# Performance work log

Hardware: AMD Instinct MI355X
Metric: run time of the kernel (lower is better)

The kernel has to match this reference:

```python
import jax, jax.numpy as jnp
import numpy as np

N = 16384      # number of nodes (pos rows)
S = 16384      # number of src nodes (src_pos rows)
E = 262144     # number of edges (COO entries)
D = 512        # embed_dim
H = 8          # num_heads
HD = D // H    # head_dim = 64
HID = 1024     # mlp hidden
MLP_IN = D + 3 * H  # 536
EPS = 1e-5


def layer_norm(x, g, b):
    mu = jnp.mean(x, axis=-1, keepdims=True)
    var = jnp.mean((x - mu) ** 2, axis=-1, keepdims=True)
    return (x - mu) * jax.lax.rsqrt(var + EPS) * g + b


def setup_inputs() -> dict:
    key = jax.random.key(0)
    ks = jax.random.split(key, 20)
    s = 1.0 / np.sqrt(D)
    sh = 1.0 / np.sqrt(HID)
    return {
        "x": jax.random.normal(ks[0], (N, D), jnp.float32),
        "Wq": jax.random.uniform(ks[1], (D, D), jnp.float32, -s, s),
        "bq": jnp.zeros((D,), jnp.float32),
        "Wk": jax.random.uniform(ks[2], (D, D), jnp.float32, -s, s),
        "bk": jnp.zeros((D,), jnp.float32),
        "g_att": jnp.ones((D,), jnp.float32),
        "b_att": jnp.zeros((D,), jnp.float32),
        "g_mlp": jnp.ones((D,), jnp.float32),
        "b_mlp": jnp.zeros((D,), jnp.float32),
        "W_in": jax.random.uniform(ks[3], (HID, MLP_IN), jnp.float32, -s, s),
        "b_in": jnp.zeros((HID,), jnp.float32),
        "W_out": jax.random.uniform(ks[4], (D, HID), jnp.float32, -sh, sh),
        "b_out": jnp.zeros((D,), jnp.float32),
        "att_bias": jax.random.normal(ks[5], (H, E), jnp.float32),
        "dist": jax.random.uniform(ks[6], (E,), jnp.float32, 0.5, 6.0),
        "pos": jax.random.normal(ks[7], (N, 3), jnp.float32),
        "src_pos": jax.random.normal(ks[8], (S, 3), jnp.float32),
        "row_index": jax.random.randint(ks[9], (E,), 0, N),
        "src_index": jax.random.randint(ks[10], (E,), 0, S),
        "org_to_src": jax.random.randint(ks[11], (S,), 0, N),
    }


def reference(x, Wq, bq, Wk, bk, g_att, b_att, g_mlp, b_mlp, W_in, b_in,
              W_out, b_out, att_bias, dist, pos, src_pos,
              row_index, src_index, org_to_src):
    n = x.shape[0]
    z = layer_norm(x, g_att, b_att)
    q = (z @ Wq.T + bq).reshape(n, H, HD)          # [N,H,hd]
    k = (z @ Wk.T + bk).reshape(n, H, HD)          # [N,H,hd]
    k_src = k[org_to_src]                          # [S,H,hd]
    # per-edge masked logits: q[row] . k_src[col] / sqrt(hd) + bias
    qe = q[row_index]                              # [E,H,hd]
    ke = k_src[src_index]                          # [E,H,hd]
    logits = jnp.einsum('ehd,ehd->eh', qe, ke) / jnp.sqrt(jnp.float32(HD))
    logits = logits + att_bias.T                   # [E,H]
    # segment (per-row) softmax over incident edges
    m = jax.ops.segment_max(logits, row_index, num_segments=n)
    p = jnp.exp(logits - m[row_index])
    den = jax.ops.segment_sum(p, row_index, num_segments=n)
    att = p / den[row_index]                       # [E,H]
    inv = jnp.where(dist == 0, 0.0, 1.0 / dist)[:, None]
    att = att * inv
    # sparse bmm: feat[h,row] += att * src_pos[col]; rowsum for centering
    sp = src_pos[src_index]                        # [E,3]
    feat = jax.ops.segment_sum(att[:, :, None] * sp[:, None, :],
                               row_index, num_segments=n)   # [N,H,3]
    rowsum = jax.ops.segment_sum(att, row_index, num_segments=n)  # [N,H]
    feat = feat - rowsum[:, :, None] * pos[:, None, :]
    feat = feat.reshape(n, H * 3)
    z2 = layer_norm(x, g_mlp, b_mlp)
    h = jax.nn.gelu(jnp.concatenate([z2, feat], axis=-1) @ W_in.T + b_in)
    return x + (h @ W_out.T + b_out)
```

## Files before the change

kernel.cpp:

```cpp
#include <hip/hip_runtime.h>
#include <math.h>


typedef unsigned short u16;
typedef __attribute__((ext_vector_type(8))) short bf16x8;
typedef __attribute__((ext_vector_type(4))) float f32x4;
typedef __attribute__((ext_vector_type(2))) float f32x2;

constexpr int N_NODES = 16384;
constexpr int E_EDGES = 262144;
constexpr int D = 512;
constexpr int KIN = 576;

constexpr size_t OFF_ZATT = 0;
constexpr size_t OFF_ZCAT = 16777216;
constexpr size_t OFF_WQK  = 35651584;
constexpr size_t OFF_BQK  = 36700160;
constexpr size_t OFF_WIN  = 36704256;
constexpr size_t OFF_WOUT = 37883904;
constexpr size_t OFF_QK   = 38932480;
constexpr size_t OFF_BKT  = 55775232;
constexpr size_t OFF_HBF  = 59969536;
constexpr size_t OFF_CNTP = 93523968;

static __device__ __forceinline__ u16 f2bf(float f) {
  union { float f; unsigned int u; } v; v.f = f;
  unsigned int u = v.u;
  u = u + 0x7FFFu + ((u >> 16) & 1u);
  return (u16)(u >> 16);
}
static __device__ __forceinline__ void gload16(const u16* g, u16* l) {
  __builtin_amdgcn_global_load_lds(
      (const __attribute__((address_space(1))) unsigned int*)g,
      (__attribute__((address_space(3))) unsigned int*)l, 16, 0, 0);
}

__global__ __launch_bounds__(256) void prep_edges(
    const int* __restrict__ row_index,
    const float* __restrict__ att_bias, const float* __restrict__ dist,
    const float* __restrict__ src_pos, const int* __restrict__ src_index,
    const int* __restrict__ org_to_src,
    int* __restrict__ cntp, int* __restrict__ bucket, float* __restrict__ rec)
{
  const int gid = blockIdx.x * 256 + threadIdx.x;
  const int r = row_index[gid];
  const int s = src_index[gid];
  const float dv = dist[gid];
  float4 q0, q1, q2, q3;
  q0.x = att_bias[gid];
  q0.y = att_bias[(size_t)1 * E_EDGES + gid];
  q0.z = att_bias[(size_t)2 * E_EDGES + gid];
  q0.w = att_bias[(size_t)3 * E_EDGES + gid];
  q1.x = att_bias[(size_t)4 * E_EDGES + gid];
  q1.y = att_bias[(size_t)5 * E_EDGES + gid];
  q1.z = att_bias[(size_t)6 * E_EDGES + gid];
  q1.w = att_bias[(size_t)7 * E_EDGES + gid];
  q2.x = (dv == 0.f) ? 0.f : 1.f / dv;
  q2.y = src_pos[(size_t)s * 3 + 0];
  q2.z = src_pos[(size_t)s * 3 + 1];
  q2.w = src_pos[(size_t)s * 3 + 2];
  q3.x = __int_as_float(org_to_src[s]);
  q3.y = 0.f; q3.z = 0.f; q3.w = 0.f;
  float4* rg = (float4*)(rec + (size_t)gid * 16);
  rg[0] = q0; rg[1] = q1; rg[2] = q2; rg[3] = q3;
  const int p = atomicAdd(&cntp[r * 16], 1);
  if (p < 64) bucket[(size_t)r * 64 + p] = gid;
}

__global__ __launch_bounds__(256) void prep_wln(
    const float* __restrict__ Wq, const float* __restrict__ Wk,
    const float* __restrict__ bq, const float* __restrict__ bk,
    const float* __restrict__ W_in, const float* __restrict__ W_out,
    u16* __restrict__ wqk, float* __restrict__ bqk,
    u16* __restrict__ win, u16* __restrict__ wout,
    const float* __restrict__ x,
    const float* __restrict__ g1, const float* __restrict__ b1,
    const float* __restrict__ g2, const float* __restrict__ b2,
    u16* __restrict__ zatt, u16* __restrict__ zcat)
{
  if (blockIdx.x < 2304) {
    const int gid = blockIdx.x * 256 + threadIdx.x;
    if (gid < 512 * 1024) {
      wqk[gid]  = f2bf(gid < 512 * 512 ? Wq[gid] : Wk[gid - 512 * 512]);
      wout[gid] = f2bf(W_out[gid]);
    }
    if (gid < 1024 * KIN) {
      const int r = gid / KIN, c = gid - r * KIN;
      win[gid] = f2bf(c < 536 ? W_in[r * 536 + c] : 0.f);
    }
    if (gid < 1024) bqk[gid] = gid < 512 ? bq[gid] : bk[gid - 512];
    return;
  }
  const int row = (blockIdx.x - 2304) * 4 + (threadIdx.x >> 6);
  const int l = threadIdx.x & 63;
  const float* xr = x + (size_t)row * D + l * 8;
  const float4 v0 = *(const float4*)(xr);
  const float4 v1 = *(const float4*)(xr + 4);
  float s  = v0.x + v0.y + v0.z + v0.w + v1.x + v1.y + v1.z + v1.w;
  float s2 = v0.x * v0.x + v0.y * v0.y + v0.z * v0.z + v0.w * v0.w
           + v1.x * v1.x + v1.y * v1.y + v1.z * v1.z + v1.w * v1.w;
#pragma unroll
  for (int m = 1; m < 64; m <<= 1) {
    s  += __shfl_xor(s, m, 64);
    s2 += __shfl_xor(s2, m, 64);
  }
  const float mu = s * (1.f / D);
  const float var = s2 * (1.f / D) - mu * mu;
  const float rs = rsqrtf(var + 1e-5f);
  const int c0 = l * 8;
  const float4 ga0 = *(const float4*)(g1 + c0), ga1 = *(const float4*)(g1 + c0 + 4);
  const float4 ba0 = *(const float4*)(b1 + c0), ba1 = *(const float4*)(b1 + c0 + 4);
  const float4 gm0 = *(const float4*)(g2 + c0), gm1 = *(const float4*)(g2 + c0 + 4);
  const float4 bm0 = *(const float4*)(b2 + c0), bm1 = *(const float4*)(b2 + c0 + 4);
  float n[8] = { (v0.x - mu) * rs, (v0.y - mu) * rs, (v0.z - mu) * rs, (v0.w - mu) * rs,
                 (v1.x - mu) * rs, (v1.y - mu) * rs, (v1.z - mu) * rs, (v1.w - mu) * rs };
  const float ga[8] = { ga0.x, ga0.y, ga0.z, ga0.w, ga1.x, ga1.y, ga1.z, ga1.w };
  const float ba[8] = { ba0.x, ba0.y, ba0.z, ba0.w, ba1.x, ba1.y, ba1.z, ba1.w };
  const float gm[8] = { gm0.x, gm0.y, gm0.z, gm0.w, gm1.x, gm1.y, gm1.z, gm1.w };
  const float bm[8] = { bm0.x, bm0.y, bm0.z, bm0.w, bm1.x, bm1.y, bm1.z, bm1.w };
  bf16x8 za, zc;
#pragma unroll
  for (int i = 0; i < 8; ++i) {
    za[i] = (short)f2bf(n[i] * ga[i] + ba[i]);
    zc[i] = (short)f2bf(n[i] * gm[i] + bm[i]);
  }
  *(bf16x8*)(zatt + (size_t)row * D + c0) = za;
  *(bf16x8*)(zcat + (size_t)row * KIN + c0) = zc;
  if (l < 32) ((unsigned int*)(zcat + (size_t)row * KIN + D))[l] = 0;
}


#define MM_BLK(AF, BF, NB) do {                                               \
  __builtin_amdgcn_s_setprio(1);                                              \
  _Pragma("unroll")                                                           \
  for (int mi = 0; mi < 8; ++mi) {                                            \
    acc[mi][NB]     = __builtin_amdgcn_mfma_f32_16x16x32_bf16(AF[mi], BF[0], acc[mi][NB], 0, 0, 0);     \
    acc[mi][NB + 1] = __builtin_amdgcn_mfma_f32_16x16x32_bf16(AF[mi], BF[1], acc[mi][NB + 1], 0, 0, 0); \
  }                                                                           \
  __builtin_amdgcn_s_setprio(0);                                              \
} while (0)

template <int EPI>
__global__ __launch_bounds__(512, 2) void gemm256(
    const u16* __restrict__ A, const u16* __restrict__ B,
    const float* __restrict__ bias,
    void* __restrict__ Cout, int M, int Nn, int K)
{
  extern __shared__ __align__(16) u16 lds[];
  const int tid = threadIdx.x;
  const int lane = tid & 63;
  const int wave = tid >> 6;
  const int wave_m = wave >> 2;
  const int wave_n = wave & 3;
  const int m0 = blockIdx.x * 256;
  const int n0 = blockIdx.y * 256;
  const int fr = lane & 15;
  const int fq = lane >> 4;
  const int NT = K >> 6;
  const int sw = (fq ^ ((fr >> 1) & 3)) * 8;

  f32x4 acc[8][4];
#pragma unroll
  for (int i = 0; i < 8; ++i)
#pragma unroll
    for (int j = 0; j < 4; ++j) acc[i][j] = 0.f;

  auto stageA = [&](int slot, int ktile, int kh) {
    u16* base = lds + slot * 8192;
    const int kb = ktile * 64 + kh * 32;
#pragma unroll
    for (int r = 0; r < 2; ++r) {
      const int g = r * 512 + tid;
      const int row = g >> 2;
      const int gs = (g & 3) ^ ((row >> 1) & 3);
      gload16(A + (size_t)(m0 + row) * K + kb + gs * 8,
              base + (r * 512 + wave * 64) * 8);
    }
  };
  auto stageB = [&](int slot, int ktile, int kh) {
    u16* base = lds + 32768 + slot * 8192;
    const int kb = ktile * 64 + kh * 32;
#pragma unroll
    for (int r = 0; r < 2; ++r) {
      const int g = r * 512 + tid;
      const int row = g >> 2;
      const int gs = (g & 3) ^ ((row >> 1) & 3);
      gload16(B + (size_t)(n0 + row) * K + kb + gs * 8,
              base + (r * 512 + wave * 64) * 8);
    }
  };
  auto ldA = [&](bf16x8 (&af)[8], int slot) {
    const u16* p = lds + slot * 8192 + (wave_m * 128 + fr) * 32 + sw;
#pragma unroll
    for (int mi = 0; mi < 8; ++mi)
      af[mi] = *(const bf16x8*)(p + mi * 16 * 32);
  };
  auto ldB = [&](bf16x8 (&bf)[2], int slot, int nh) {
    const u16* p = lds + 32768 + slot * 8192 + (wave_n * 64 + nh * 32 + fr) * 32 + sw;
    bf[0] = *(const bf16x8*)(p);
    bf[1] = *(const bf16x8*)(p + 16 * 32);
  };

  stageA(0, 0, 0); stageB(0, 0, 0);
  stageA(1, 0, 1); stageB(1, 0, 1);
  stageA(2, 1, 0); stageB(2, 1, 0);
  stageA(3, 1, 1);
  asm volatile("s_waitcnt vmcnt(10)" ::: "memory");
  __builtin_amdgcn_s_barrier();
  asm volatile("" ::: "memory");

  bf16x8 af[8], bf0[2], bf1[2];
  for (int t = 0; t < NT; ++t) {
    const int sa0 = (2 * t) & 3,  sa1 = (2 * t + 1) & 3;
    const int sb1n = (2 * t + 3) & 3;
    const int t1 = (t + 1 >= NT) ? t + 1 - NT : t + 1;
    const int t2 = (t + 2 >= NT) ? t + 2 - NT : t + 2;

    ldA(af, sa0); ldB(bf0, sa0, 0);
    stageB(sb1n, t1, 1);
    __builtin_amdgcn_s_barrier();
    asm volatile("" ::: "memory");
    MM_BLK(af, bf0, 0);
    __builtin_amdgcn_s_barrier();
    asm volatile("" ::: "memory");
    ldB(bf1, sa0, 1);
    stageA(sa0, t2, 0);
    __builtin_amdgcn_s_barrier();
    asm volatile("" ::: "memory");
    MM_BLK(af, bf1, 2);
    asm volatile("s_waitcnt vmcnt(10)" ::: "memory");
    __builtin_amdgcn_s_barrier();
    asm volatile("" ::: "memory");
    ldA(af, sa1); ldB(bf0, sa1, 0);
    stageB(sa0, t2, 0);
    __builtin_amdgcn_s_barrier();
    asm volatile("" ::: "memory");
    MM_BLK(af, bf0, 0);
    __builtin_amdgcn_s_barrier();
    asm volatile("" ::: "memory");
    ldB(bf1, sa1, 1);
    stageA(sa1, t2, 1);
    __builtin_amdgcn_s_barrier();
    asm volatile("" ::: "memory");
    MM_BLK(af, bf1, 2);
    asm volatile("s_waitcnt vmcnt(10)" ::: "memory");
    __builtin_amdgcn_s_barrier();
    asm volatile("" ::: "memory");
  }
  asm volatile("s_waitcnt vmcnt(0)" ::: "memory");

#pragma unroll
  for (int mi = 0; mi < 8; ++mi) {
#pragma unroll
    for (int nj = 0; nj < 4; ++nj) {
      const int col = n0 + wave_n * 64 + nj * 16 + fr;
      const float bv = bias[col];
#pragma unroll
      for (int rr = 0; rr < 4; ++rr) {
        const int row = m0 + wave_m * 128 + mi * 16 + fq * 4 + rr;
        float v = acc[mi][nj][rr] + bv;
        if (EPI == 1) {
          const float nu = -1.5957691216057308f * (v + 0.044715f * v * v * v);
          const float sg = __builtin_amdgcn_rcpf(1.f + __expf(nu));
          ((u16*)Cout)[(size_t)row * Nn + col] = f2bf(v * sg);
        } else {
          const int pk = __builtin_amdgcn_cvt_pk_fp8_f32(v, v, 0, false);
          ((unsigned char*)Cout)[(size_t)row * Nn + col] = (unsigned char)(pk & 0xFF);
        }
      }
    }
  }
}

template <int EPI, int WPE>
__global__ __launch_bounds__(256, WPE) void gemm_nt(
    const u16* __restrict__ A, const u16* __restrict__ B,
    const float* __restrict__ bias, const float* __restrict__ resid,
    void* __restrict__ Cout, int M, int Nn, int K)
{
  constexpr int BM = 128, BN = 128, BK = 32;
  __shared__ __align__(16) u16 As[2 * BM * BK];
  __shared__ __align__(16) u16 Bs[2 * BN * BK];
  const int tid = threadIdx.x;
  const int lane = tid & 63;
  const int wave = tid >> 6;
  const int m0 = blockIdx.x * BM;
  const int n0 = blockIdx.y * BN;
  const int wm = (wave >> 1) * 64;
  const int wn = (wave & 1) * 64;
  const int fr = lane & 15;
  const int fq = lane >> 4;
  const int srow = lane >> 2;
  const int skoff = ((lane & 3) ^ ((srow >> 1) & 3)) * 8;
  const int sw = (fq ^ ((fr >> 1) & 3)) * 8;

  f32x4 acc[4][4];
#pragma unroll
  for (int i = 0; i < 4; ++i)
#pragma unroll
    for (int j = 0; j < 4; ++j) acc[i][j] = 0.f;

  for (int k0 = 0; k0 < K; k0 += 2 * BK) {
    __syncthreads();
#pragma unroll
    for (int t = 0; t < 2; ++t) {
#pragma unroll
      for (int r = 0; r < 2; ++r) {
        const int rowbase = r * 64 + wave * 16;
        gload16(A + (size_t)(m0 + rowbase + srow) * K + k0 + t * BK + skoff,
                As + t * (BM * BK) + rowbase * BK);
        gload16(B + (size_t)(n0 + rowbase + srow) * K + k0 + t * BK + skoff,
                Bs + t * (BM * BK) + rowbase * BK);
      }
    }
    __syncthreads();
#pragma unroll
    for (int t = 0; t < 2; ++t) {
      bf16x8 af[4], bfr[4];
#pragma unroll
      for (int mi = 0; mi < 4; ++mi)
        af[mi] = *(const bf16x8*)(As + t * (BM * BK) + (wm + mi * 16 + fr) * BK + sw);
#pragma unroll
      for (int ni = 0; ni < 4; ++ni)
        bfr[ni] = *(const bf16x8*)(Bs + t * (BM * BK) + (wn + ni * 16 + fr) * BK + sw);
#pragma unroll
      for (int mi = 0; mi < 4; ++mi)
#pragma unroll
        for (int ni = 0; ni < 4; ++ni)
          acc[mi][ni] = __builtin_amdgcn_mfma_f32_16x16x32_bf16(af[mi], bfr[ni], acc[mi][ni], 0, 0, 0);
    }
  }

#pragma unroll
  for (int mi = 0; mi < 4; ++mi) {
#pragma unroll
    for (int ni = 0; ni < 4; ++ni) {
      const int col = n0 + wn + ni * 16 + fr;
      const float bv = bias[col];
#pragma unroll
      for (int rr = 0; rr < 4; ++rr) {
        const int row = m0 + wm + mi * 16 + fq * 4 + rr;
        float v = acc[mi][ni][rr] + bv;
        if (EPI == 1) {
          const float nu = -1.5957691216057308f * (v + 0.044715f * v * v * v);
          const float sg = __builtin_amdgcn_rcpf(1.f + __expf(nu));
          ((u16*)Cout)[(size_t)row * Nn + col] = f2bf(v * sg);
        } else if (EPI == 2) {
          ((float*)Cout)[(size_t)row * Nn + col] = v + resid[(size_t)row * Nn + col];
        } else {
          const int pk = __builtin_amdgcn_cvt_pk_fp8_f32(v, v, 0, false);
          ((unsigned char*)Cout)[(size_t)row * Nn + col] = (unsigned char)(pk & 0xFF);
        }
      }
    }
  }
}

__global__ __launch_bounds__(256) void edge_csr(
    const unsigned char* __restrict__ qk8, const float* __restrict__ rec,
    const int* __restrict__ cntp, const int* __restrict__ bucket,
    const float* __restrict__ pos, u16* __restrict__ zcat)
{
  const int lane = threadIdx.x & 63;
  const int wave = threadIdx.x >> 6;
  const int row = blockIdx.x * 4 + wave;
  const int half = lane >> 5;
  const int sub = lane & 31;
  const int h = sub >> 2, j = sub & 3;
  const int deg = min(cntp[row * 16], 64);
  const int base = row * 64;

  const uint4 qv = *(const uint4*)(qk8 + (size_t)row * 1024 + sub * 16);
  float qf[16];
  {
    const unsigned int* qu = (const unsigned int*)&qv;
#pragma unroll
    for (int i = 0; i < 4; ++i) {
      const f32x2 lo = __builtin_amdgcn_cvt_pk_f32_fp8(qu[i], false);
      const f32x2 hi = __builtin_amdgcn_cvt_pk_f32_fp8(qu[i], true);
      qf[i * 4 + 0] = lo.x; qf[i * 4 + 1] = lo.y;
      qf[i * 4 + 2] = hi.x; qf[i * 4 + 3] = hi.y;
    }
  }

  float accA = 0.f, accB = 0.f;
  const int npair = (deg + 1) >> 1;

  bool ok0 = half < deg;
  int e0 = ok0 ? bucket[base + half] : 0;
  const float* r0 = rec + (size_t)e0 * 16;
  float bias0 = r0[h], invd0 = r0[8];
  float spA0 = (j >= 2) ? r0[7 + j] : 0.f;
  float spB0 = (j == 1) ? r0[11] : 0.f;
  uint4 kv0 = *(const uint4*)(qk8 + (size_t)__float_as_int(r0[12]) * 1024 + 512 + sub * 16);

  bool ok1 = 2 + half < deg;
  int e1 = ok1 ? bucket[base + 2 + half] : 0;
  const float* r1 = rec + (size_t)e1 * 16;
  float bias1 = r1[h], invd1 = r1[8];
  float spA1 = (j >= 2) ? r1[7 + j] : 0.f;
  float spB1 = (j == 1) ? r1[11] : 0.f;
  uint4 kv1 = *(const uint4*)(qk8 + (size_t)__float_as_int(r1[12]) * 1024 + 512 + sub * 16);

  bool ok2 = 4 + half < deg;
  int e2 = ok2 ? bucket[base + 4 + half] : 0;
  const float* r2p = rec + (size_t)e2 * 16;
  float bias2 = r2p[h], invd2 = r2p[8];
  float spA2 = (j >= 2) ? r2p[7 + j] : 0.f;
  float spB2 = (j == 1) ? r2p[11] : 0.f;
  int kr2 = __float_as_int(r2p[12]);

  bool ok3 = 6 + half < deg;
  int e3 = ok3 ? bucket[base + 6 + half] : 0;

  for (int i = 0; i < npair; ++i) {
    const uint4 kv2 = *(const uint4*)(qk8 + (size_t)kr2 * 1024 + 512 + sub * 16);
    const float* r3 = rec + (size_t)e3 * 16;
    const float bias3 = r3[h], invd3 = r3[8];
    const float spA3 = (j >= 2) ? r3[7 + j] : 0.f;
    const float spB3 = (j == 1) ? r3[11] : 0.f;
    const int kr3 = __float_as_int(r3[12]);
    const bool ok4 = 2 * (i + 4) + half < deg;
    const int e4 = ok4 ? bucket[base + 2 * (i + 4) + half] : 0;

    float p;
    {
      const unsigned int* ku = (const unsigned int*)&kv0;
      const f32x2 a0 = __builtin_amdgcn_cvt_pk_f32_fp8(ku[0], false);
      const f32x2 a1 = __builtin_amdgcn_cvt_pk_f32_fp8(ku[0], true);
      const f32x2 b0 = __builtin_amdgcn_cvt_pk_f32_fp8(ku[1], false);
      const f32x2 b1 = __builtin_amdgcn_cvt_pk_f32_fp8(ku[1], true);
      const f32x2 c0 = __builtin_amdgcn_cvt_pk_f32_fp8(ku[2], false);
      const f32x2 c1 = __builtin_amdgcn_cvt_pk_f32_fp8(ku[2], true);
      const f32x2 d0 = __builtin_amdgcn_cvt_pk_f32_fp8(ku[3], false);
      const f32x2 d1 = __builtin_amdgcn_cvt_pk_f32_fp8(ku[3], true);
      p = qf[0] * a0.x;
      p = fmaf(qf[1],  a0.y, p);  p = fmaf(qf[2],  a1.x, p);  p = fmaf(qf[3],  a1.y, p);
      p = fmaf(qf[4],  b0.x, p);  p = fmaf(qf[5],  b0.y, p);  p = fmaf(qf[6],  b1.x, p);
      p = fmaf(qf[7],  b1.y, p);  p = fmaf(qf[8],  c0.x, p);  p = fmaf(qf[9],  c0.y, p);
      p = fmaf(qf[10], c1.x, p);  p = fmaf(qf[11], c1.y, p);  p = fmaf(qf[12], d0.x, p);
      p = fmaf(qf[13], d0.y, p);  p = fmaf(qf[14], d1.x, p);  p = fmaf(qf[15], d1.y, p);
    }
    p += __shfl_xor(p, 1, 64);
    p += __shfl_xor(p, 2, 64);
    float pe = __expf(p * 0.125f + bias0);
    pe = ok0 ? pe : 0.f;
    const float w = pe * invd0;
    accA += (j == 0) ? pe : (j == 1) ? w : w * spA0;
    accB += w * spB0;

    ok0 = ok1; bias0 = bias1; invd0 = invd1; spA0 = spA1; spB0 = spB1; kv0 = kv1;
    ok1 = ok2; bias1 = bias2; invd1 = invd2; spA1 = spA2; spB1 = spB2; kv1 = kv2;
    ok2 = ok3; bias2 = bias3; invd2 = invd3; spA2 = spA3; spB2 = spB3; kr2 = kr3;
    ok3 = ok4; e3 = e4;
  }

  accA += __shfl_xor(accA, 32, 64);
  accB += __shfl_xor(accB, 32, 64);
  const int hb = h << 2;
  const float den  = __shfl(accA, hb + 0, 64);
  const float wsum = __shfl(accA, hb + 1, 64);
  const float wsp01 = __shfl(accA, hb + 2 + (j & 1), 64);
  const float wsp2  = __shfl(accB, hb + 1, 64);
  const float invd = (den != 0.f) ? 1.f / den : 0.f;
  const float rsum = wsum * invd;
  if (half == 0 && j < 3) {
    const float wspj = (j < 2) ? wsp01 : wsp2;
    zcat[(size_t)row * KIN + D + h * 3 + j] = f2bf(wspj * invd - rsum * pos[row * 3 + j]);
  }
}

extern "C" void kernel_launch(void* const* d_in, const int* in_sizes, int n_in,
                              void* d_out, int out_size, void* d_ws, size_t ws_size,
                              hipStream_t stream)
{
  const float* x        = (const float*)d_in[0];
  const float* Wq       = (const float*)d_in[1];
  const float* bq       = (const float*)d_in[2];
  const float* Wk       = (const float*)d_in[3];
  const float* bk       = (const float*)d_in[4];
  const float* g_att    = (const float*)d_in[5];
  const float* b_att    = (const float*)d_in[6];
  const float* g_mlp    = (const float*)d_in[7];
  const float* b_mlp    = (const float*)d_in[8];
  const float* W_in     = (const float*)d_in[9];
  const float* b_in     = (const float*)d_in[10];
  const float* W_out    = (const float*)d_in[11];
  const float* b_out    = (const float*)d_in[12];
  const float* att_bias = (const float*)d_in[13];
  const float* dist     = (const float*)d_in[14];
  const float* pos      = (const float*)d_in[15];
  const float* src_pos  = (const float*)d_in[16];
  const int* row_index  = (const int*)d_in[17];
  const int* src_index  = (const int*)d_in[18];
  const int* org_to_src = (const int*)d_in[19];

  char* ws = (char*)d_ws;
  u16*   zatt = (u16*)(ws + OFF_ZATT);
  u16*   zcat = (u16*)(ws + OFF_ZCAT);
  u16*   wqk  = (u16*)(ws + OFF_WQK);
  float* bqk  = (float*)(ws + OFF_BQK);
  u16*   win  = (u16*)(ws + OFF_WIN);
  u16*   wout = (u16*)(ws + OFF_WOUT);
  unsigned char* qk8 = (unsigned char*)(ws + OFF_QK);
  int*   bkt  = (int*)(ws + OFF_BKT);
  u16*   hbf  = (u16*)(ws + OFF_HBF);
  float* rec  = (float*)(ws + OFF_HBF);
  int*   cntp = (int*)(ws + OFF_CNTP);

  static bool s_attr = false;
  if (!s_attr) {
    hipFuncSetAttribute(reinterpret_cast<const void*>(&gemm256<4>),
                        hipFuncAttributeMaxDynamicSharedMemorySize, 131072);
    hipFuncSetAttribute(reinterpret_cast<const void*>(&gemm256<1>),
                        hipFuncAttributeMaxDynamicSharedMemorySize, 131072);
    s_attr = true;
  }

  hipMemsetAsync(ws + OFF_CNTP, 0, 16384 * 64, stream);

  prep_edges<<<E_EDGES / 256, 256, 0, stream>>>(
      row_index, att_bias, dist, src_pos, src_index, org_to_src, cntp, bkt, rec);
  prep_wln<<<2304 + N_NODES / 4, 256, 0, stream>>>(
      Wq, Wk, bq, bk, W_in, W_out, wqk, bqk, win, wout,
      x, g_att, b_att, g_mlp, b_mlp, zatt, zcat);
  gemm256<4><<<dim3(64, 4), 512, 131072, stream>>>(zatt, wqk, bqk, qk8, N_NODES, 1024, 512);
  edge_csr<<<N_NODES / 4, 256, 0, stream>>>(qk8, rec, cntp, bkt, pos, zcat);
  gemm256<1><<<dim3(64, 4), 512, 131072, stream>>>(zcat, win, b_in, hbf, N_NODES, 1024, KIN);
  gemm_nt<2, 2><<<dim3(128, 4), 256, 0, stream>>>(hbf, wout, b_out, x, d_out, N_NODES, 512, 1024);
}
```

Before: 256.5 us.

## Fuse MLP up and down projections into one kernel keeping hidden in LDS

Replaces the two separate MLP GEMM launches with a single kernel. Each 64-row block computes the GELU hidden activations into shared memory and then immediately multiplies by W_out, adding bias and residual. This avoids writing and re-reading the full bf16 hidden tensor through global memory and saves a launch. In exchange it uses about 144KB of LDS per block, which limits occupancy to one block per CU, and weight operands are streamed from global/L2 into registers without LDS staging.

```diff
diff --git a/kernel.cpp b/kernel.cpp
--- a/kernel.cpp
+++ b/kernel.cpp
@@ -20,7 +20,7 @@
 constexpr size_t OFF_WOUT = 37883904;
 constexpr size_t OFF_QK   = 38932480;
 constexpr size_t OFF_BKT  = 55775232;
-constexpr size_t OFF_HBF  = 59969536;
+constexpr size_t OFF_REC  = 59969536;
 constexpr size_t OFF_CNTP = 93523968;
 
 static __device__ __forceinline__ u16 f2bf(float f) {
@@ -129,7 +129,6 @@
   if (l < 32) ((unsigned int*)(zcat + (size_t)row * KIN + D))[l] = 0;
 }
 
-
 #define MM_BLK(AF, BF, NB) do {                                               \
   __builtin_amdgcn_s_setprio(1);                                              \
   _Pragma("unroll")                                                           \
@@ -272,88 +271,169 @@
   }
 }
 
-template <int EPI, int WPE>
-__global__ __launch_bounds__(256, WPE) void gemm_nt(
-    const u16* __restrict__ A, const u16* __restrict__ B,
-    const float* __restrict__ bias, const float* __restrict__ resid,
-    void* __restrict__ Cout, int M, int Nn, int K)
+__global__ __launch_bounds__(512, 2) void gemm23(
+    const u16* __restrict__ zcat, const u16* __restrict__ win,
+    const float* __restrict__ b_in, const u16* __restrict__ wout,
+    const float* __restrict__ b_out, const float* __restrict__ x,
+    float* __restrict__ out)
 {
-  constexpr int BM = 128, BN = 128, BK = 32;
-  __shared__ __align__(16) u16 As[2 * BM * BK];
-  __shared__ __align__(16) u16 Bs[2 * BN * BK];
+  extern __shared__ __align__(16) u16 lds[];
+  u16* As = lds;
+  u16* Hs = lds + 8192;
   const int tid = threadIdx.x;
   const int lane = tid & 63;
-  const int wave = tid >> 6;
-  const int m0 = blockIdx.x * BM;
-  const int n0 = blockIdx.y * BN;
-  const int wm = (wave >> 1) * 64;
-  const int wn = (wave & 1) * 64;
+  const int wv = tid >> 6;
   const int fr = lane & 15;
   const int fq = lane >> 4;
-  const int srow = lane >> 2;
-  const int skoff = ((lane & 3) ^ ((srow >> 1) & 3)) * 8;
-  const int sw = (fq ^ ((fr >> 1) & 3)) * 8;
-
-  f32x4 acc[4][4];
+  const int m0 = blockIdx.x * 64;
+
+  f32x4 acc[4][8];
 #pragma unroll
   for (int i = 0; i < 4; ++i)
 #pragma unroll
-    for (int j = 0; j < 4; ++j) acc[i][j] = 0.f;
-
-  for (int k0 = 0; k0 < K; k0 += 2 * BK) {
-    __syncthreads();
-#pragma unroll
-    for (int t = 0; t < 2; ++t) {
-#pragma unroll
-      for (int r = 0; r < 2; ++r) {
-        const int rowbase = r * 64 + wave * 16;
-        gload16(A + (size_t)(m0 + rowbase + srow) * K + k0 + t * BK + skoff,
-                As + t * (BM * BK) + rowbase * BK);
-        gload16(B + (size_t)(n0 + rowbase + srow) * K + k0 + t * BK + skoff,
-                Bs + t * (BM * BK) + rowbase * BK);
-      }
-    }
-    __syncthreads();
-#pragma unroll
-    for (int t = 0; t < 2; ++t) {
-      bf16x8 af[4], bfr[4];
-#pragma unroll
-      for (int mi = 0; mi < 4; ++mi)
-        af[mi] = *(const bf16x8*)(As + t * (BM * BK) + (wm + mi * 16 + fr) * BK + sw);
-#pragma unroll
-      for (int ni = 0; ni < 4; ++ni)
-        bfr[ni] = *(const bf16x8*)(Bs + t * (BM * BK) + (wn + ni * 16 + fr) * BK + sw);
-#pragma unroll
-      for (int mi = 0; mi < 4; ++mi)
-#pragma unroll
-        for (int ni = 0; ni < 4; ++ni)
-          acc[mi][ni] = __builtin_amdgcn_mfma_f32_16x16x32_bf16(af[mi], bfr[ni], acc[mi][ni], 0, 0, 0);
-    }
-  }
-
-#pragma unroll
-  for (int mi = 0; mi < 4; ++mi) {
-#pragma unroll
-    for (int ni = 0; ni < 4; ++ni) {
-      const int col = n0 + wn + ni * 16 + fr;
-      const float bv = bias[col];
-#pragma unroll
-      for (int rr = 0; rr < 4; ++rr) {
-        const int row = m0 + wm + mi * 16 + fq * 4 + rr;
-        float v = acc[mi][ni][rr] + bv;
-        if (EPI == 1) {
+    for (int j = 0; j < 8; ++j) acc[i][j] = 0.f;
+
+  auto stA = [&](int t, int slot) {
+    const int row = tid >> 3, gd = tid & 7;
+    const int gs = gd ^ (row & 7);
+    gload16(zcat + (size_t)(m0 + row) * KIN + t * 64 + gs * 8,
+            As + slot * 4096 + (wv * 64 + lane) * 8);
+  };
+  auto ldAfr = [&](int slot, int kk, int mi) -> bf16x8 {
+    const int row = mi * 16 + fr;
+    const int g = (kk * 4 + fq) ^ (fr & 7);
+    return *(const bf16x8*)(As + slot * 4096 + row * 64 + g * 8);
+  };
+  auto ldBin = [&](int t, int kk, int nj) -> bf16x8 {
+    return *(const bf16x8*)(win + (size_t)(wv * 128 + nj * 16 + fr) * KIN
+                            + t * 64 + kk * 32 + fq * 8);
+  };
+
+  bf16x8 bA[8], bB[8], a2[4];
+  stA(0, 0);
+#pragma unroll
+  for (int nj = 0; nj < 8; ++nj) bA[nj] = ldBin(0, 0, nj);
+  asm volatile("s_waitcnt vmcnt(8)" ::: "memory");
+  __builtin_amdgcn_s_barrier();
+  asm volatile("" ::: "memory");
+
+#pragma unroll
+  for (int t = 0; t < 9; ++t) {
+    const int slot = t & 1;
+    if (t < 8) stA(t + 1, slot ^ 1);
+    __builtin_amdgcn_sched_barrier(0);
+#pragma unroll
+    for (int nj = 0; nj < 8; ++nj) bB[nj] = ldBin(t, 1, nj);
+#pragma unroll
+    for (int mi = 0; mi < 4; ++mi) a2[mi] = ldAfr(slot, 0, mi);
+    __builtin_amdgcn_s_setprio(1);
+#pragma unroll
+    for (int mi = 0; mi < 4; ++mi)
+#pragma unroll
+      for (int nj = 0; nj < 8; ++nj)
+        acc[mi][nj] = __builtin_amdgcn_mfma_f32_16x16x32_bf16(a2[mi], bA[nj], acc[mi][nj], 0, 0, 0);
+    __builtin_amdgcn_s_setprio(0);
+    if (t < 8) {
+#pragma unroll
+      for (int nj = 0; nj < 8; ++nj) bA[nj] = ldBin(t + 1, 0, nj);
+    }
+#pragma unroll
+    for (int mi = 0; mi < 4; ++mi) a2[mi] = ldAfr(slot, 1, mi);
+    __builtin_amdgcn_s_setprio(1);
+#pragma unroll
+    for (int mi = 0; mi < 4; ++mi)
+#pragma unroll
+      for (int nj = 0; nj < 8; ++nj)
+        acc[mi][nj] = __builtin_amdgcn_mfma_f32_16x16x32_bf16(a2[mi], bB[nj], acc[mi][nj], 0, 0, 0);
+    __builtin_amdgcn_s_setprio(0);
+    if (t < 8) {
+      asm volatile("s_waitcnt vmcnt(8)" ::: "memory");
+      __builtin_amdgcn_s_barrier();
+      asm volatile("" ::: "memory");
+    }
+  }
+
+  {
+    float bvv[8];
+#pragma unroll
+    for (int nj = 0; nj < 8; ++nj) bvv[nj] = b_in[wv * 128 + nj * 16 + fr];
+#pragma unroll
+    for (int mi = 0; mi < 4; ++mi)
+#pragma unroll
+      for (int nj = 0; nj < 8; ++nj) {
+        const int col = wv * 128 + nj * 16 + fr;
+        const int colg = col >> 3, cr = col & 7;
+#pragma unroll
+        for (int rr = 0; rr < 4; ++rr) {
+          const int row = mi * 16 + fq * 4 + rr;
+          float v = acc[mi][nj][rr] + bvv[nj];
           const float nu = -1.5957691216057308f * (v + 0.044715f * v * v * v);
           const float sg = __builtin_amdgcn_rcpf(1.f + __expf(nu));
-          ((u16*)Cout)[(size_t)row * Nn + col] = f2bf(v * sg);
-        } else if (EPI == 2) {
-          ((float*)Cout)[(size_t)row * Nn + col] = v + resid[(size_t)row * Nn + col];
-        } else {
-          const int pk = __builtin_amdgcn_cvt_pk_fp8_f32(v, v, 0, false);
-          ((unsigned char*)Cout)[(size_t)row * Nn + col] = (unsigned char)(pk & 0xFF);
+          Hs[row * 1024 + ((colg ^ (row & 7)) * 8) + cr] = f2bf(v * sg);
         }
       }
-    }
-  }
+  }
+  __syncthreads();
+
+  f32x4 o[4][4];
+#pragma unroll
+  for (int i = 0; i < 4; ++i)
+#pragma unroll
+    for (int j = 0; j < 4; ++j) o[i][j] = 0.f;
+
+  auto ldH = [&](int ks, int mi) -> bf16x8 {
+    const int row = mi * 16 + fr;
+    const int g = (ks * 4 + fq) ^ (fr & 7);
+    return *(const bf16x8*)(Hs + row * 1024 + g * 8);
+  };
+  auto ldBo = [&](int ks, int nj) -> bf16x8 {
+    return *(const bf16x8*)(wout + (size_t)(wv * 64 + nj * 16 + fr) * 1024
+                            + ks * 32 + fq * 8);
+  };
+
+  bf16x8 oA[4], oB[4], ha[4];
+#pragma unroll
+  for (int nj = 0; nj < 4; ++nj) oA[nj] = ldBo(0, nj);
+#pragma unroll
+  for (int ks = 0; ks < 32; ks += 2) {
+#pragma unroll
+    for (int nj = 0; nj < 4; ++nj) oB[nj] = ldBo(ks + 1, nj);
+#pragma unroll
+    for (int mi = 0; mi < 4; ++mi) ha[mi] = ldH(ks, mi);
+    __builtin_amdgcn_s_setprio(1);
+#pragma unroll
+    for (int mi = 0; mi < 4; ++mi)
+#pragma unroll
+      for (int nj = 0; nj < 4; ++nj)
+        o[mi][nj] = __builtin_amdgcn_mfma_f32_16x16x32_bf16(ha[mi], oA[nj], o[mi][nj], 0, 0, 0);
+    __builtin_amdgcn_s_setprio(0);
+    if (ks + 2 < 32) {
+#pragma unroll
+      for (int nj = 0; nj < 4; ++nj) oA[nj] = ldBo(ks + 2, nj);
+    }
+#pragma unroll
+    for (int mi = 0; mi < 4; ++mi) ha[mi] = ldH(ks + 1, mi);
+    __builtin_amdgcn_s_setprio(1);
+#pragma unroll
+    for (int mi = 0; mi < 4; ++mi)
+#pragma unroll
+      for (int nj = 0; nj < 4; ++nj)
+        o[mi][nj] = __builtin_amdgcn_mfma_f32_16x16x32_bf16(ha[mi], oB[nj], o[mi][nj], 0, 0, 0);
+    __builtin_amdgcn_s_setprio(0);
+  }
+
+#pragma unroll
+  for (int mi = 0; mi < 4; ++mi)
+#pragma unroll
+    for (int nj = 0; nj < 4; ++nj) {
+      const int col = wv * 64 + nj * 16 + fr;
+      const float bv = b_out[col];
+#pragma unroll
+      for (int rr = 0; rr < 4; ++rr) {
+        const int row = m0 + mi * 16 + fq * 4 + rr;
+        out[(size_t)row * 512 + col] = o[mi][nj][rr] + bv + x[(size_t)row * 512 + col];
+      }
+    }
 }
 
 __global__ __launch_bounds__(256) void edge_csr(
@@ -504,16 +584,15 @@
   u16*   wout = (u16*)(ws + OFF_WOUT);
   unsigned char* qk8 = (unsigned char*)(ws + OFF_QK);
   int*   bkt  = (int*)(ws + OFF_BKT);
-  u16*   hbf  = (u16*)(ws + OFF_HBF);
-  float* rec  = (float*)(ws + OFF_HBF);
+  float* rec  = (float*)(ws + OFF_REC);
   int*   cntp = (int*)(ws + OFF_CNTP);
 
   static bool s_attr = false;
   if (!s_attr) {
     hipFuncSetAttribute(reinterpret_cast<const void*>(&gemm256<4>),
                         hipFuncAttributeMaxDynamicSharedMemorySize, 131072);
-    hipFuncSetAttribute(reinterpret_cast<const void*>(&gemm256<1>),
-                        hipFuncAttributeMaxDynamicSharedMemorySize, 131072);
+    hipFuncSetAttribute(reinterpret_cast<const void*>(&gemm23),
+                        hipFuncAttributeMaxDynamicSharedMemorySize, 147456);
     s_attr = true;
   }
 
@@ -526,6 +605,5 @@
       x, g_att, b_att, g_mlp, b_mlp, zatt, zcat);
   gemm256<4><<<dim3(64, 4), 512, 131072, stream>>>(zatt, wqk, bqk, qk8, N_NODES, 1024, 512);
   edge_csr<<<N_NODES / 4, 256, 0, stream>>>(qk8, rec, cntp, bkt, pos, zcat);
-  gemm256<1><<<dim3(64, 4), 512, 131072, stream>>>(zcat, win, b_in, hbf, N_NODES, 1024, KIN);
-  gemm_nt<2, 2><<<dim3(128, 4), 256, 0, stream>>>(hbf, wout, b_out, x, d_out, N_NODES, 512, 1024);
-}
+  gemm23<<<N_NODES / 64, 512, 147456, stream>>>(zcat, win, b_in, wout, b_out, x, (float*)d_out);
+}
```

Result: slower. 275.9 us (+7.6%).

## Merge edge and weight prep kernels; pipelined 256x128 tile for output GEMM

Applied to the files above, without the earlier changes.

Fuses prep_edges and prep_wln into a single prep_all launch, giving the edge records their own workspace region so they no longer alias the hidden buffer. Replaces the 128x128 double-buffered output-projection GEMM with a 512-thread 256x128-tile kernel that uses a four-slot LDS pipeline, split barriers and vmcnt waits, following the structure of gemm256. The aim is fewer launches and better MFMA utilisation with load/compute overlap in the final GEMM. The cost is more LDS per block and fewer blocks (256) for 256 CUs, plus prefetch that wraps around to tile 0 and issues redundant loads.

```diff
diff --git a/kernel.cpp b/kernel.cpp
--- a/kernel.cpp
+++ b/kernel.cpp
@@ -21,7 +21,8 @@
 constexpr size_t OFF_QK   = 38932480;
 constexpr size_t OFF_BKT  = 55775232;
 constexpr size_t OFF_HBF  = 59969536;
-constexpr size_t OFF_CNTP = 93523968;
+constexpr size_t OFF_REC  = 93523968;
+constexpr size_t OFF_CNTP = 110301184;
 
 static __device__ __forceinline__ u16 f2bf(float f) {
   union { float f; unsigned int u; } v; v.f = f;
@@ -35,39 +36,12 @@
       (__attribute__((address_space(3))) unsigned int*)l, 16, 0, 0);
 }
 
-__global__ __launch_bounds__(256) void prep_edges(
+__global__ __launch_bounds__(256) void prep_all(
     const int* __restrict__ row_index,
     const float* __restrict__ att_bias, const float* __restrict__ dist,
     const float* __restrict__ src_pos, const int* __restrict__ src_index,
     const int* __restrict__ org_to_src,
-    int* __restrict__ cntp, int* __restrict__ bucket, float* __restrict__ rec)
-{
-  const int gid = blockIdx.x * 256 + threadIdx.x;
-  const int r = row_index[gid];
-  const int s = src_index[gid];
-  const float dv = dist[gid];
-  float4 q0, q1, q2, q3;
-  q0.x = att_bias[gid];
-  q0.y = att_bias[(size_t)1 * E_EDGES + gid];
-  q0.z = att_bias[(size_t)2 * E_EDGES + gid];
-  q0.w = att_bias[(size_t)3 * E_EDGES + gid];
-  q1.x = att_bias[(size_t)4 * E_EDGES + gid];
-  q1.y = att_bias[(size_t)5 * E_EDGES + gid];
-  q1.z = att_bias[(size_t)6 * E_EDGES + gid];
-  q1.w = att_bias[(size_t)7 * E_EDGES + gid];
-  q2.x = (dv == 0.f) ? 0.f : 1.f / dv;
-  q2.y = src_pos[(size_t)s * 3 + 0];
-  q2.z = src_pos[(size_t)s * 3 + 1];
-  q2.w = src_pos[(size_t)s * 3 + 2];
-  q3.x = __int_as_float(org_to_src[s]);
-  q3.y = 0.f; q3.z = 0.f; q3.w = 0.f;
-  float4* rg = (float4*)(rec + (size_t)gid * 16);
-  rg[0] = q0; rg[1] = q1; rg[2] = q2; rg[3] = q3;
-  const int p = atomicAdd(&cntp[r * 16], 1);
-  if (p < 64) bucket[(size_t)r * 64 + p] = gid;
-}
-
-__global__ __launch_bounds__(256) void prep_wln(
+    int* __restrict__ cntp, int* __restrict__ bucket, float* __restrict__ rec,
     const float* __restrict__ Wq, const float* __restrict__ Wk,
     const float* __restrict__ bq, const float* __restrict__ bk,
     const float* __restrict__ W_in, const float* __restrict__ W_out,
@@ -78,8 +52,34 @@
     const float* __restrict__ g2, const float* __restrict__ b2,
     u16* __restrict__ zatt, u16* __restrict__ zcat)
 {
-  if (blockIdx.x < 2304) {
+  if (blockIdx.x < 1024) {
     const int gid = blockIdx.x * 256 + threadIdx.x;
+    const int r = row_index[gid];
+    const int s = src_index[gid];
+    const float dv = dist[gid];
+    float4 q0, q1, q2, q3;
+    q0.x = att_bias[gid];
+    q0.y = att_bias[(size_t)1 * E_EDGES + gid];
+    q0.z = att_bias[(size_t)2 * E_EDGES + gid];
+    q0.w = att_bias[(size_t)3 * E_EDGES + gid];
+    q1.x = att_bias[(size_t)4 * E_EDGES + gid];
+    q1.y = att_bias[(size_t)5 * E_EDGES + gid];
+    q1.z = att_bias[(size_t)6 * E_EDGES + gid];
+    q1.w = att_bias[(size_t)7 * E_EDGES + gid];
+    q2.x = (dv == 0.f) ? 0.f : 1.f / dv;
+    q2.y = src_pos[(size_t)s * 3 + 0];
+    q2.z = src_pos[(size_t)s * 3 + 1];
+    q2.w = src_pos[(size_t)s * 3 + 2];
+    q3.x = __int_as_float(org_to_src[s]);
+    q3.y = 0.f; q3.z = 0.f; q3.w = 0.f;
+    float4* rg = (float4*)(rec + (size_t)gid * 16);
+    rg[0] = q0; rg[1] = q1; rg[2] = q2; rg[3] = q3;
+    const int p = atomicAdd(&cntp[r * 16], 1);
+    if (p < 64) bucket[(size_t)r * 64 + p] = gid;
+    return;
+  }
+  if (blockIdx.x < 3328) {
+    const int gid = (blockIdx.x - 1024) * 256 + threadIdx.x;
     if (gid < 512 * 1024) {
       wqk[gid]  = f2bf(gid < 512 * 512 ? Wq[gid] : Wk[gid - 512 * 512]);
       wout[gid] = f2bf(W_out[gid]);
@@ -91,7 +91,7 @@
     if (gid < 1024) bqk[gid] = gid < 512 ? bq[gid] : bk[gid - 512];
     return;
   }
-  const int row = (blockIdx.x - 2304) * 4 + (threadIdx.x >> 6);
+  const int row = (blockIdx.x - 3328) * 4 + (threadIdx.x >> 6);
   const int l = threadIdx.x & 63;
   const float* xr = x + (size_t)row * D + l * 8;
   const float4 v0 = *(const float4*)(xr);
@@ -128,7 +128,6 @@
   *(bf16x8*)(zcat + (size_t)row * KIN + c0) = zc;
   if (l < 32) ((unsigned int*)(zcat + (size_t)row * KIN + D))[l] = 0;
 }
-
 
 #define MM_BLK(AF, BF, NB) do {                                               \
   __builtin_amdgcn_s_setprio(1);                                              \
@@ -272,85 +271,103 @@
   }
 }
 
-template <int EPI, int WPE>
-__global__ __launch_bounds__(256, WPE) void gemm_nt(
+__global__ __launch_bounds__(512, 2) void gemm_mlp(
     const u16* __restrict__ A, const u16* __restrict__ B,
     const float* __restrict__ bias, const float* __restrict__ resid,
-    void* __restrict__ Cout, int M, int Nn, int K)
+    float* __restrict__ Cout, int M, int Nn, int K)
 {
-  constexpr int BM = 128, BN = 128, BK = 32;
-  __shared__ __align__(16) u16 As[2 * BM * BK];
-  __shared__ __align__(16) u16 Bs[2 * BN * BK];
+  extern __shared__ __align__(16) u16 lds[];
   const int tid = threadIdx.x;
   const int lane = tid & 63;
   const int wave = tid >> 6;
-  const int m0 = blockIdx.x * BM;
-  const int n0 = blockIdx.y * BN;
-  const int wm = (wave >> 1) * 64;
-  const int wn = (wave & 1) * 64;
+  const int wave_m = wave >> 2;
+  const int wave_n = wave & 3;
+  const int m0 = blockIdx.x * 256;
+  const int n0 = blockIdx.y * 128;
   const int fr = lane & 15;
   const int fq = lane >> 4;
-  const int srow = lane >> 2;
-  const int skoff = ((lane & 3) ^ ((srow >> 1) & 3)) * 8;
+  const int NT = K >> 6;
   const int sw = (fq ^ ((fr >> 1) & 3)) * 8;
 
-  f32x4 acc[4][4];
-#pragma unroll
-  for (int i = 0; i < 4; ++i)
-#pragma unroll
-    for (int j = 0; j < 4; ++j) acc[i][j] = 0.f;
-
-  for (int k0 = 0; k0 < K; k0 += 2 * BK) {
-    __syncthreads();
-#pragma unroll
-    for (int t = 0; t < 2; ++t) {
-#pragma unroll
-      for (int r = 0; r < 2; ++r) {
-        const int rowbase = r * 64 + wave * 16;
-        gload16(A + (size_t)(m0 + rowbase + srow) * K + k0 + t * BK + skoff,
-                As + t * (BM * BK) + rowbase * BK);
-        gload16(B + (size_t)(n0 + rowbase + srow) * K + k0 + t * BK + skoff,
-                Bs + t * (BM * BK) + rowbase * BK);
-      }
-    }
-    __syncthreads();
-#pragma unroll
-    for (int t = 0; t < 2; ++t) {
-      bf16x8 af[4], bfr[4];
-#pragma unroll
-      for (int mi = 0; mi < 4; ++mi)
-        af[mi] = *(const bf16x8*)(As + t * (BM * BK) + (wm + mi * 16 + fr) * BK + sw);
-#pragma unroll
-      for (int ni = 0; ni < 4; ++ni)
-        bfr[ni] = *(const bf16x8*)(Bs + t * (BM * BK) + (wn + ni * 16 + fr) * BK + sw);
-#pragma unroll
-      for (int mi = 0; mi < 4; ++mi)
-#pragma unroll
-        for (int ni = 0; ni < 4; ++ni)
-          acc[mi][ni] = __builtin_amdgcn_mfma_f32_16x16x32_bf16(af[mi], bfr[ni], acc[mi][ni], 0, 0, 0);
-    }
-  }
-
-#pragma unroll
-  for (int mi = 0; mi < 4; ++mi) {
-#pragma unroll
-    for (int ni = 0; ni < 4; ++ni) {
-      const int col = n0 + wn + ni * 16 + fr;
+  f32x4 acc[8][2];
+#pragma unroll
+  for (int i = 0; i < 8; ++i) { acc[i][0] = 0.f; acc[i][1] = 0.f; }
+
+  auto stageA = [&](int slot, int ktile, int kh) {
+    u16* base = lds + slot * 8192;
+    const int kb = ktile * 64 + kh * 32;
+#pragma unroll
+    for (int r = 0; r < 2; ++r) {
+      const int g = r * 512 + tid;
+      const int row = g >> 2;
+      const int gs = (g & 3) ^ ((row >> 1) & 3);
+      gload16(A + (size_t)(m0 + row) * K + kb + gs * 8,
+              base + (r * 512 + wave * 64) * 8);
+    }
+  };
+  auto stageB = [&](int slot, int ktile, int kh) {
+    u16* base = lds + 32768 + slot * 4096;
+    const int kb = ktile * 64 + kh * 32;
+    const int row = tid >> 2;
+    const int gs = (tid & 3) ^ ((row >> 1) & 3);
+    gload16(B + (size_t)(n0 + row) * K + kb + gs * 8,
+            base + (wave * 64 + lane) * 8);
+  };
+  auto ldA = [&](bf16x8 (&af)[8], int slot) {
+    const u16* p = lds + slot * 8192 + (wave_m * 128 + fr) * 32 + sw;
+#pragma unroll
+    for (int mi = 0; mi < 8; ++mi)
+      af[mi] = *(const bf16x8*)(p + mi * 16 * 32);
+  };
+  auto ldB2 = [&](bf16x8 (&bf)[2], int slot) {
+    const u16* p = lds + 32768 + slot * 4096 + (wave_n * 32 + fr) * 32 + sw;
+    bf[0] = *(const bf16x8*)(p);
+    bf[1] = *(const bf16x8*)(p + 16 * 32);
+  };
+
+  stageA(0, 0, 0); stageB(0, 0, 0);
+  stageA(1, 0, 1); stageB(1, 0, 1);
+  stageA(2, 1, 0); stageB(2, 1, 0);
+  asm volatile("s_waitcnt vmcnt(6)" ::: "memory");
+  __builtin_amdgcn_s_barrier();
+  asm volatile("" ::: "memory");
+
+  bf16x8 af[8], bf[2];
+  for (int t = 0; t < NT; ++t) {
+    const int sa0 = (2 * t) & 3, sa1 = (2 * t + 1) & 3;
+    const int sn  = (2 * t + 3) & 3;
+    const int t1 = (t + 1 >= NT) ? t + 1 - NT : t + 1;
+    const int t2 = (t + 2 >= NT) ? t + 2 - NT : t + 2;
+
+    ldA(af, sa0); ldB2(bf, sa0);
+    stageA(sn, t1, 1); stageB(sn, t1, 1);
+    __builtin_amdgcn_s_barrier();
+    asm volatile("" ::: "memory");
+    MM_BLK(af, bf, 0);
+    asm volatile("s_waitcnt vmcnt(6)" ::: "memory");
+    __builtin_amdgcn_s_barrier();
+    asm volatile("" ::: "memory");
+    ldA(af, sa1); ldB2(bf, sa1);
+    stageA(sa0, t2, 0); stageB(sa0, t2, 0);
+    __builtin_amdgcn_s_barrier();
+    asm volatile("" ::: "memory");
+    MM_BLK(af, bf, 0);
+    asm volatile("s_waitcnt vmcnt(6)" ::: "memory");
+    __builtin_amdgcn_s_barrier();
+    asm volatile("" ::: "memory");
+  }
+  asm volatile("s_waitcnt vmcnt(0)" ::: "memory");
+
+#pragma unroll
+  for (int mi = 0; mi < 8; ++mi) {
+#pragma unroll
+    for (int nj = 0; nj < 2; ++nj) {
+      const int col = n0 + wave_n * 32 + nj * 16 + fr;
       const float bv = bias[col];
 #pragma unroll
       for (int rr = 0; rr < 4; ++rr) {
-        const int row = m0 + wm + mi * 16 + fq * 4 + rr;
-        float v = acc[mi][ni][rr] + bv;
-        if (EPI == 1) {
-          const float nu = -1.5957691216057308f * (v + 0.044715f * v * v * v);
-          const float sg = __builtin_amdgcn_rcpf(1.f + __expf(nu));
-          ((u16*)Cout)[(size_t)row * Nn + col] = f2bf(v * sg);
-        } else if (EPI == 2) {
-          ((float*)Cout)[(size_t)row * Nn + col] = v + resid[(size_t)row * Nn + col];
-        } else {
-          const int pk = __builtin_amdgcn_cvt_pk_fp8_f32(v, v, 0, false);
-          ((unsigned char*)Cout)[(size_t)row * Nn + col] = (unsigned char)(pk & 0xFF);
-        }
+        const int row = m0 + wave_m * 128 + mi * 16 + fq * 4 + rr;
+        Cout[(size_t)row * Nn + col] = acc[mi][nj][rr] + bv + resid[(size_t)row * Nn + col];
       }
     }
   }
@@ -505,7 +522,7 @@
   unsigned char* qk8 = (unsigned char*)(ws + OFF_QK);
   int*   bkt  = (int*)(ws + OFF_BKT);
   u16*   hbf  = (u16*)(ws + OFF_HBF);
-  float* rec  = (float*)(ws + OFF_HBF);
+  float* rec  = (float*)(ws + OFF_REC);
   int*   cntp = (int*)(ws + OFF_CNTP);
 
   static bool s_attr = false;
@@ -514,18 +531,19 @@
                         hipFuncAttributeMaxDynamicSharedMemorySize, 131072);
     hipFuncSetAttribute(reinterpret_cast<const void*>(&gemm256<1>),
                         hipFuncAttributeMaxDynamicSharedMemorySize, 131072);
+    hipFuncSetAttribute(reinterpret_cast<const void*>(&gemm_mlp),
+                        hipFuncAttributeMaxDynamicSharedMemorySize, 98304);
     s_attr = true;
   }
 
   hipMemsetAsync(ws + OFF_CNTP, 0, 16384 * 64, stream);
 
-  prep_edges<<<E_EDGES / 256, 256, 0, stream>>>(
-      row_index, att_bias, dist, src_pos, src_index, org_to_src, cntp, bkt, rec);
-  prep_wln<<<2304 + N_NODES / 4, 256, 0, stream>>>(
+  prep_all<<<1024 + 2304 + N_NODES / 4, 256, 0, stream>>>(
+      row_index, att_bias, dist, src_pos, src_index, org_to_src, cntp, bkt, rec,
       Wq, Wk, bq, bk, W_in, W_out, wqk, bqk, win, wout,
       x, g_att, b_att, g_mlp, b_mlp, zatt, zcat);
   gemm256<4><<<dim3(64, 4), 512, 131072, stream>>>(zatt, wqk, bqk, qk8, N_NODES, 1024, 512);
   edge_csr<<<N_NODES / 4, 256, 0, stream>>>(qk8, rec, cntp, bkt, pos, zcat);
   gemm256<1><<<dim3(64, 4), 512, 131072, stream>>>(zcat, win, b_in, hbf, N_NODES, 1024, KIN);
-  gemm_nt<2, 2><<<dim3(128, 4), 256, 0, stream>>>(hbf, wout, b_out, x, d_out, N_NODES, 512, 1024);
-}
+  gemm_mlp<<<dim3(64, 4), 512, 98304, stream>>>(hbf, wout, b_out, x, (float*)d_out, N_NODES, 512, 1024);
+}
```

Measured after the change: 254.6 us. Within noise of the previous version (-0.8%).
